# Kernel optimization log

Hardware: AMD Instinct MI355X
Metric: run time of the kernel (lower is better)

## Reference

```python
import jax, jax.numpy as jnp
import numpy as np

B, S, H, NH = 2, 2048, 1024, 16
HD = H // NH


def setup_inputs() -> dict:
    key = jax.random.key(0)
    ks = jax.random.split(key, 12)
    inp = {
        "query": jax.random.normal(ks[0], (B, S, H), dtype=jnp.float32),
        "key": jax.random.normal(ks[1], (B, S, H), dtype=jnp.float32),
        "value": jax.random.normal(ks[2], (B, S, H), dtype=jnp.float32),
        "mask": jnp.ones((B, 1, S, S), dtype=jnp.int32),
        "script_mask": jax.random.uniform(ks[3], (B, S, S), dtype=jnp.float32),
    }
    scale = 1.0 / np.sqrt(H)
    inp["Wq"] = jax.random.normal(ks[4], (H, H), dtype=jnp.float32) * scale
    inp["bq"] = jnp.zeros((H,), dtype=jnp.float32)
    inp["Wk"] = jax.random.normal(ks[5], (H, H), dtype=jnp.float32) * scale
    inp["bk"] = jnp.zeros((H,), dtype=jnp.float32)
    inp["Wv"] = jax.random.normal(ks[6], (H, H), dtype=jnp.float32) * scale
    inp["bv"] = jnp.zeros((H,), dtype=jnp.float32)
    inp["Wo"] = jax.random.normal(ks[7], (H, H), dtype=jnp.float32) * scale
    inp["bo"] = jnp.zeros((H,), dtype=jnp.float32)
    return inp


def reference(query, key, value, mask, script_mask, Wq, bq, Wk, bk, Wv, bv, Wo, bo):
    b, s, h = query.shape
    # projections; torch Linear: x @ W.T + b
    q = (query @ Wq.T + bq).reshape(b, s, NH, HD).transpose(0, 2, 1, 3)  # [b,nh,s,hd]
    k = (key @ Wk.T + bk).reshape(b, s, NH, HD).transpose(0, 2, 1, 3)
    v = (value @ Wv.T + bv).reshape(b, s, NH, HD).transpose(0, 2, 1, 3)
    scores = jnp.einsum("bhqd,bhkd->bhqk", q, k) / jnp.sqrt(jnp.float32(HD))
    # multiplicative script mask, broadcast over heads
    scores = scores * script_mask[:, None, :, :]
    # additive mask: positions where mask == 0 -> -inf
    scores = jnp.where(mask == 0, -jnp.inf, scores)
    attn = jax.nn.softmax(scores, axis=-1)
    out = jnp.einsum("bhqk,bhkd->bhqd", attn, v)  # [b,nh,s,hd]
    out = out.transpose(0, 2, 1, 3).reshape(b, s, h)
    return out @ Wo.T + bo
```

## Files before the change

kernel.cpp:

```cpp
#include <hip/hip_runtime.h>
#include <stdint.h>

#define NH 16
#define SEQ 2048
#define HDIM 1024

typedef short bf16x8 __attribute__((ext_vector_type(8)));
typedef float f32x4 __attribute__((ext_vector_type(4)));

#define NEG_BIG (-1.0e30f)

static __device__ __forceinline__ float bf2f(uint32_t u) {
  union { uint32_t u; float f; } v; v.u = u << 16; return v.f;
}
static __device__ __forceinline__ uint32_t cvtpk_bf16(float lo, float hi) {
  uint32_t r;
  asm("v_cvt_pk_bf16_f32 %0, %1, %2" : "=v"(r) : "v"(lo), "v"(hi));
  return r;
}
static __device__ __forceinline__ uint16_t f2bf(float f) {
  return (uint16_t)cvtpk_bf16(f, f);
}
static __device__ __forceinline__ void gload_lds16(const void* g, void* l) {
  __builtin_amdgcn_global_load_lds(
      (const __attribute__((address_space(1))) void*)g,
      (__attribute__((address_space(3))) void*)l, 16, 0, 0);
}

struct CvtArgs {
  const float* src[7];
  uint16_t* dst[7];
  int nblk[7];
};
__global__ __launch_bounds__(256) void cvt_bf16(CvtArgs a) {
  int ten = blockIdx.y;
  if (blockIdx.x >= a.nblk[ten]) return;
  size_t idx = ((size_t)blockIdx.x * 256 + threadIdx.x) * 8;
  const float* s = a.src[ten] + idx;
  float4 f0 = *(const float4*)(s);
  float4 f1 = *(const float4*)(s + 4);
  uint4 o;
  o.x = cvtpk_bf16(f0.x, f0.y);
  o.y = cvtpk_bf16(f0.z, f0.w);
  o.z = cvtpk_bf16(f1.x, f1.y);
  o.w = cvtpk_bf16(f1.z, f1.w);
  *(uint4*)(a.dst[ten] + idx) = o;
}

__global__ __launch_bounds__(256) void cm_prep(const int4* __restrict__ mask,
                                               const float4* __restrict__ sm,
                                               uint4* __restrict__ cm) {
  int i = blockIdx.x * 256 + threadIdx.x;
  int4 m0 = mask[2 * i];
  int4 m1 = mask[2 * i + 1];
  float4 s0 = sm[2 * i];
  float4 s1 = sm[2 * i + 1];
  const float cst = 0.18033688011112042f;
  auto pk = [&](int mA, int mB, float fa, float fb) -> uint32_t {
    float a = mA ? fa * cst : -1.0f;
    float b = mB ? fb * cst : -1.0f;
    return cvtpk_bf16(a, b);
  };
  uint4 o;
  o.x = pk(m0.x, m0.y, s0.x, s0.y);
  o.y = pk(m0.z, m0.w, s0.z, s0.w);
  o.z = pk(m1.x, m1.y, s1.x, s1.y);
  o.w = pk(m1.z, m1.w, s1.z, s1.w);
  cm[i] = o;
}

struct GemmArgs {
  const uint16_t* A[4];
  const uint16_t* B[4];
  const float* bias[4];
  void* C[4];
};

__global__ __launch_bounds__(256) void gemm_bt(GemmArgs ga, int modeBase) {
  int mode = modeBase + blockIdx.y;
  const uint16_t* __restrict__ A = ga.A[mode];
  const uint16_t* __restrict__ Bm = ga.B[mode];
  const float* __restrict__ bias = ga.bias[mode];

  int bid = blockIdx.x;
  int tm, tn;
  if (mode == 2) { tm = bid & 7; tn = bid >> 3; }
  else           { tm = bid >> 3; tn = bid & 7; }

  __shared__ uint16_t As[3][128 * 32];
  __shared__ uint16_t Bs[3][128 * 32];

  int t = threadIdx.x;
  int lane = t & 63, w = t >> 6;
  int quad = lane >> 4, lm = lane & 15;
  int wm = w >> 1, wn = w & 1;

  const uint16_t* Ab = A + (size_t)tm * 128 * 1024;
  const uint16_t* Bb = Bm + (size_t)tn * 128 * 1024;

  int srow = lane >> 2;
  int scol = (lane & 3) * 8;
  const uint16_t* gA0 = Ab + (size_t)(w * 32 + srow) * 1024 + scol;
  const uint16_t* gA1 = gA0 + 16 * 1024;
  const uint16_t* gB0 = Bb + (size_t)(w * 32 + srow) * 1024 + scol;
  const uint16_t* gB1 = gB0 + 16 * 1024;

  uint16_t* rdA = As[0]; uint16_t* stA = As[1]; uint16_t* nxA = As[2];
  uint16_t* rdB = Bs[0]; uint16_t* stB = Bs[1]; uint16_t* nxB = Bs[2];
  int woff = w * 1024;

  auto STAGE = [&](uint16_t* dA, uint16_t* dB) {
    gload_lds16(gA0, dA + woff);
    gload_lds16(gA1, dA + woff + 512);
    gload_lds16(gB0, dB + woff);
    gload_lds16(gB1, dB + woff + 512);
    gA0 += 32; gA1 += 32; gB0 += 32; gB1 += 32;
  };

  f32x4 acc[4][4] = {};

  STAGE(rdA, rdB);

  for (int kk = 0; kk < 1024; kk += 32) {
    if (kk + 32 < 1024) {
      STAGE(stA, stB);
      asm volatile("s_waitcnt vmcnt(4)" ::: "memory");
    } else {
      asm volatile("s_waitcnt vmcnt(0)" ::: "memory");
    }
    __builtin_amdgcn_s_barrier();
    __builtin_amdgcn_sched_barrier(0);

    bf16x8 af[4], bfr[4];
#pragma unroll
    for (int i = 0; i < 4; i++)
      af[i] = *(const bf16x8*)&rdA[(wm * 64 + i * 16 + lm) * 32 + quad * 8];
#pragma unroll
    for (int j = 0; j < 4; j++)
      bfr[j] = *(const bf16x8*)&rdB[(wn * 64 + j * 16 + lm) * 32 + quad * 8];
#pragma unroll
    for (int i = 0; i < 4; i++)
#pragma unroll
      for (int j = 0; j < 4; j++)
        acc[i][j] = __builtin_amdgcn_mfma_f32_16x16x32_bf16(af[i], bfr[j], acc[i][j], 0, 0, 0);

    uint16_t* tA = rdA; rdA = stA; stA = nxA; nxA = tA;
    uint16_t* tB = rdB; rdB = stB; stB = nxB; nxB = tB;
  }

  int rowb = tm * 128 + wm * 64;
  int colb = tn * 128 + wn * 64;
#pragma unroll
  for (int i = 0; i < 4; i++) {
#pragma unroll
    for (int j = 0; j < 4; j++) {
      int col = colb + j * 16 + lm;
#pragma unroll
      for (int r = 0; r < 4; r++) {
        int row = rowb + i * 16 + quad * 4 + r;
        float v = acc[i][j][r];
        if (mode == 2) {
          v += bias[row];
          int hh = row >> 6, hd = row & 63, b = col >> 11, s2 = col & 2047;
          ((uint16_t*)ga.C[2])[((size_t)((b * NH + hh) * 64 + hd) << 11) + s2] = f2bf(v);
        } else if (mode == 3) {
          v += bias[col];
          ((float*)ga.C[3])[(size_t)row * 1024 + col] = v;
        } else {
          v += bias[col];
          int b = row >> 11, s2 = row & 2047, hh = col >> 6, hd = col & 63;
          ((uint16_t*)ga.C[mode])[(((size_t)(b * NH + hh) * 2048 + s2) << 6) + hd] = f2bf(v);
        }
      }
    }
  }
}

#define LDK 72

__global__ __launch_bounds__(256) void attn(const uint16_t* __restrict__ qp,
                                            const uint16_t* __restrict__ kp,
                                            const uint16_t* __restrict__ vt,
                                            const uint16_t* __restrict__ cm,
                                            uint16_t* __restrict__ ao) {
  int h = blockIdx.x, qt = blockIdx.y, b = blockIdx.z;
  int t = threadIdx.x;
  int lane = t & 63, w = t >> 6;
  int quad = lane >> 4, c = lane & 15;

  __shared__ uint16_t Ks[64 * LDK];
  __shared__ uint16_t VTs[64 * LDK];
  __shared__ uint16_t Ps[64 * LDK];

  size_t bh = (size_t)(b * NH + h);
  const uint16_t* Kb = kp + bh * (SEQ * 64);
  const uint16_t* Vb = vt + bh * (64 * SEQ);
  const uint16_t* CMb = cm + ((size_t)b * SEQ + qt * 64) * SEQ;

  int qrow = qt * 64 + w * 16 + c;
  const uint16_t* Qb = qp + bh * (SEQ * 64) + (size_t)qrow * 64;
  bf16x8 qf0 = *(const bf16x8*)(Qb + quad * 8);
  bf16x8 qf1 = *(const bf16x8*)(Qb + 32 + quad * 8);

  f32x4 Oacc[4] = {};
  float m_run = NEG_BIG;
  float l_run = 0.0f;

  int krow = w * 8 + (lane >> 3);
  int kc = (lane & 7) * 8;

  const uint16_t* pK0 = Kb + (size_t)krow * 64 + kc;
  const uint16_t* pK1 = pK0 + 32 * 64;
  const uint16_t* pV0 = Vb + (size_t)krow * SEQ + kc;
  const uint16_t* pV1 = pV0 + (size_t)32 * SEQ;
  const uint16_t* pCM = CMb + (size_t)(w * 16 + c) * SEQ + quad * 4;

  uint16_t* sK0 = &Ks[krow * LDK + kc];
  uint16_t* sK1 = sK0 + 32 * LDK;
  uint16_t* sV0 = &VTs[krow * LDK + kc];
  uint16_t* sV1 = sV0 + 32 * LDK;

  const uint16_t* rK = &Ks[c * LDK];
  const uint16_t* rV = &VTs[c * LDK];
  uint16_t* sP = &Ps[(w * 16 + c) * LDK];
  int qo = quad * 8;

  for (int kt = 0; kt < SEQ; kt += 64) {
    uint2 cm0 = *(const uint2*)(pCM);
    uint2 cm1 = *(const uint2*)(pCM + 16);
    uint2 cm2 = *(const uint2*)(pCM + 32);
    uint2 cm3 = *(const uint2*)(pCM + 48);
    uint4 k0  = *(const uint4*)(pK0);
    uint4 k1  = *(const uint4*)(pK1);
    uint4 v0g = *(const uint4*)(pV0);
    uint4 v1g = *(const uint4*)(pV1);
    pCM += 64; pK0 += 64 * 64; pK1 += 64 * 64; pV0 += 64; pV1 += 64;
    __syncthreads();
    *(uint4*)sK0 = k0;
    *(uint4*)sK1 = k1;
    *(uint4*)sV0 = v0g;
    *(uint4*)sV1 = v1g;
    __syncthreads();

    f32x4 st[4];
    __builtin_amdgcn_s_setprio(1);
#pragma unroll
    for (int i = 0; i < 4; i++) {
      bf16x8 a0 = *(const bf16x8*)(rK + i * 16 * LDK + qo);
      bf16x8 a1 = *(const bf16x8*)(rK + i * 16 * LDK + 32 + qo);
      f32x4 z = {};
      z = __builtin_amdgcn_mfma_f32_16x16x32_bf16(a0, qf0, z, 0, 0, 0);
      st[i] = __builtin_amdgcn_mfma_f32_16x16x32_bf16(a1, qf1, z, 0, 0, 0);
    }
    __builtin_amdgcn_s_setprio(0);

    float p[16];
    float tmax = NEG_BIG;
    uint2 cmv[4] = {cm0, cm1, cm2, cm3};
#pragma unroll
    for (int i = 0; i < 4; i++) {
      uint32_t w0 = cmv[i].x, w1 = cmv[i].y;
      float cf[4];
      cf[0] = __builtin_bit_cast(float, w0 << 16);
      cf[1] = __builtin_bit_cast(float, w0 & 0xffff0000u);
      cf[2] = __builtin_bit_cast(float, w1 << 16);
      cf[3] = __builtin_bit_cast(float, w1 & 0xffff0000u);
#pragma unroll
      for (int r = 0; r < 4; r++) {
        float sv = st[i][r] * cf[r];
        sv = (cf[r] < 0.0f) ? NEG_BIG : sv;
        p[i * 4 + r] = sv;
      }
      tmax = fmaxf(tmax,
                   fmaxf(fmaxf(p[i * 4 + 0], p[i * 4 + 1]),
                         fmaxf(p[i * 4 + 2], p[i * 4 + 3])));
    }
    tmax = fmaxf(tmax, __shfl_xor(tmax, 16));
    tmax = fmaxf(tmax, __shfl_xor(tmax, 32));
    if (!__all(tmax <= m_run + 8.0f)) {
      float m_new = fmaxf(m_run, tmax);
      float alpha = exp2f(m_run - m_new);
      m_run = m_new;
      l_run *= alpha;
#pragma unroll
      for (int i = 0; i < 4; i++) Oacc[i] *= alpha;
    }
    float ls = 0.0f;
#pragma unroll
    for (int z2 = 0; z2 < 16; z2++) {
      p[z2] = exp2f(p[z2] - m_run);
      ls += p[z2];
    }
    l_run += ls;

#pragma unroll
    for (int i = 0; i < 4; i++) {
      uint2 pkd;
      pkd.x = cvtpk_bf16(p[i * 4 + 0], p[i * 4 + 1]);
      pkd.y = cvtpk_bf16(p[i * 4 + 2], p[i * 4 + 3]);
      *(uint2*)(sP + i * 16 + quad * 4) = pkd;
    }
    asm volatile("s_waitcnt lgkmcnt(0)" ::: "memory");
    __builtin_amdgcn_sched_barrier(0);

    bf16x8 pf0 = *(const bf16x8*)(sP + qo);
    bf16x8 pf1 = *(const bf16x8*)(sP + 32 + qo);
    __builtin_amdgcn_s_setprio(1);
#pragma unroll
    for (int i = 0; i < 4; i++) {
      bf16x8 v0 = *(const bf16x8*)(rV + i * 16 * LDK + qo);
      bf16x8 v1 = *(const bf16x8*)(rV + i * 16 * LDK + 32 + qo);
      Oacc[i] = __builtin_amdgcn_mfma_f32_16x16x32_bf16(v0, pf0, Oacc[i], 0, 0, 0);
      Oacc[i] = __builtin_amdgcn_mfma_f32_16x16x32_bf16(v1, pf1, Oacc[i], 0, 0, 0);
    }
    __builtin_amdgcn_s_setprio(0);
  }

  float lf = l_run + __shfl_xor(l_run, 16);
  lf = lf + __shfl_xor(lf, 32);
  float inv = 1.0f / lf;
  uint16_t* Ob = ao + ((size_t)(b * SEQ) + qt * 64 + w * 16 + c) * HDIM + h * 64;
#pragma unroll
  for (int i = 0; i < 4; i++) {
    uint2 ov;
    ov.x = cvtpk_bf16(Oacc[i][0] * inv, Oacc[i][1] * inv);
    ov.y = cvtpk_bf16(Oacc[i][2] * inv, Oacc[i][3] * inv);
    *(uint2*)(Ob + i * 16 + quad * 4) = ov;
  }
}

extern "C" void kernel_launch(void* const* d_in, const int* in_sizes, int n_in,
                              void* d_out, int out_size, void* d_ws, size_t ws_size,
                              hipStream_t stream) {
  (void)in_sizes; (void)n_in; (void)out_size; (void)ws_size;
  const float* query = (const float*)d_in[0];
  const float* key   = (const float*)d_in[1];
  const float* value = (const float*)d_in[2];
  const int*   mask  = (const int*)d_in[3];
  const float* smask = (const float*)d_in[4];
  const float* Wq = (const float*)d_in[5];
  const float* bq = (const float*)d_in[6];
  const float* Wk = (const float*)d_in[7];
  const float* bk = (const float*)d_in[8];
  const float* Wv = (const float*)d_in[9];
  const float* bv = (const float*)d_in[10];
  const float* Wo = (const float*)d_in[11];
  const float* bo = (const float*)d_in[12];

  char* p = (char*)d_ws;
  uint16_t* xq  = (uint16_t*)p; p += (size_t)2 * SEQ * HDIM * 2;
  uint16_t* xk  = (uint16_t*)p; p += (size_t)2 * SEQ * HDIM * 2;
  uint16_t* xv  = (uint16_t*)p; p += (size_t)2 * SEQ * HDIM * 2;
  uint16_t* wqb = (uint16_t*)p; p += (size_t)HDIM * HDIM * 2;
  uint16_t* wkb = (uint16_t*)p; p += (size_t)HDIM * HDIM * 2;
  uint16_t* wvb = (uint16_t*)p; p += (size_t)HDIM * HDIM * 2;
  uint16_t* wob = (uint16_t*)p; p += (size_t)HDIM * HDIM * 2;
  uint16_t* qp  = (uint16_t*)p; p += (size_t)2 * NH * SEQ * 64 * 2;
  uint16_t* kpp = (uint16_t*)p; p += (size_t)2 * NH * SEQ * 64 * 2;
  uint16_t* vtp = (uint16_t*)p; p += (size_t)2 * NH * SEQ * 64 * 2;
  uint16_t* cmw = (uint16_t*)p; p += (size_t)2 * SEQ * SEQ * 2;
  uint16_t* aob = (uint16_t*)p; p += (size_t)2 * SEQ * HDIM * 2;

  CvtArgs ca;
  ca.src[0] = query; ca.dst[0] = xq;  ca.nblk[0] = 2048;
  ca.src[1] = key;   ca.dst[1] = xk;  ca.nblk[1] = 2048;
  ca.src[2] = value; ca.dst[2] = xv;  ca.nblk[2] = 2048;
  ca.src[3] = Wq;    ca.dst[3] = wqb; ca.nblk[3] = 512;
  ca.src[4] = Wk;    ca.dst[4] = wkb; ca.nblk[4] = 512;
  ca.src[5] = Wv;    ca.dst[5] = wvb; ca.nblk[5] = 512;
  ca.src[6] = Wo;    ca.dst[6] = wob; ca.nblk[6] = 512;
  cvt_bf16<<<dim3(2048, 7), 256, 0, stream>>>(ca);

  cm_prep<<<4096, 256, 0, stream>>>((const int4*)mask, (const float4*)smask, (uint4*)cmw);

  GemmArgs ga;
  ga.A[0] = xq;  ga.B[0] = wqb; ga.bias[0] = bq; ga.C[0] = qp;
  ga.A[1] = xk;  ga.B[1] = wkb; ga.bias[1] = bk; ga.C[1] = kpp;
  ga.A[2] = wvb; ga.B[2] = xv;  ga.bias[2] = bv; ga.C[2] = vtp;
  ga.A[3] = aob; ga.B[3] = wob; ga.bias[3] = bo; ga.C[3] = d_out;

  gemm_bt<<<dim3(256, 3), 256, 0, stream>>>(ga, 0);
  attn<<<dim3(NH, SEQ / 64, 2), 256, 0, stream>>>(qp, kpp, vtp, cmw, aob);
  gemm_bt<<<dim3(256, 1), 256, 0, stream>>>(ga, 3);
}
```

Baseline: 343.2 us.

## Double-buffer K/V tiles in attention and add smaller-tile output GEMM

The attention kernel now double-buffers its K and V shared-memory tiles. The next tile's global loads are issued before the current tile's compute and written to the alternate buffer afterward, which leaves one barrier per iteration instead of two. The output projection moves to a dedicated kernel with 64x128 tiles and 512 blocks, raising occupancy across CUs for the 4096x1024 GEMM. The cost is more LDS per attention block, which may reduce occupancy, and more registers held across the loop.

```diff
diff --git a/kernel.cpp b/kernel.cpp
--- a/kernel.cpp
+++ b/kernel.cpp
@@ -10,9 +10,6 @@
 
 #define NEG_BIG (-1.0e30f)
 
-static __device__ __forceinline__ float bf2f(uint32_t u) {
-  union { uint32_t u; float f; } v; v.u = u << 16; return v.f;
-}
 static __device__ __forceinline__ uint32_t cvtpk_bf16(float lo, float hi) {
   uint32_t r;
   asm("v_cvt_pk_bf16_f32 %0, %1, %2" : "=v"(r) : "v"(lo), "v"(hi));
@@ -163,9 +160,6 @@
           v += bias[row];
           int hh = row >> 6, hd = row & 63, b = col >> 11, s2 = col & 2047;
           ((uint16_t*)ga.C[2])[((size_t)((b * NH + hh) * 64 + hd) << 11) + s2] = f2bf(v);
-        } else if (mode == 3) {
-          v += bias[col];
-          ((float*)ga.C[3])[(size_t)row * 1024 + col] = v;
         } else {
           v += bias[col];
           int b = row >> 11, s2 = row & 2047, hh = col >> 6, hd = col & 63;
@@ -176,7 +170,93 @@
   }
 }
 
+__global__ __launch_bounds__(256) void gemm_out(const uint16_t* __restrict__ A,
+                                                const uint16_t* __restrict__ Bm,
+                                                const float* __restrict__ bias,
+                                                float* __restrict__ C) {
+  int bid = blockIdx.x;
+  int tm = bid >> 3;
+  int tn = bid & 7;
+
+  __shared__ uint16_t As[3][64 * 32];
+  __shared__ uint16_t Bs[3][128 * 32];
+
+  int t = threadIdx.x;
+  int lane = t & 63, w = t >> 6;
+  int quad = lane >> 4, lm = lane & 15;
+  int wm = w >> 1, wn = w & 1;
+
+  const uint16_t* Ab = A + (size_t)tm * 64 * 1024;
+  const uint16_t* Bb = Bm + (size_t)tn * 128 * 1024;
+
+  int srow = lane >> 2;
+  int scol = (lane & 3) * 8;
+  const uint16_t* gA0 = Ab + (size_t)(w * 16 + srow) * 1024 + scol;
+  const uint16_t* gB0 = Bb + (size_t)(w * 32 + srow) * 1024 + scol;
+  const uint16_t* gB1 = gB0 + 16 * 1024;
+
+  uint16_t* rdA = As[0]; uint16_t* stA = As[1]; uint16_t* nxA = As[2];
+  uint16_t* rdB = Bs[0]; uint16_t* stB = Bs[1]; uint16_t* nxB = Bs[2];
+  int woffA = w * 512;
+  int woffB = w * 1024;
+
+  auto STAGE = [&](uint16_t* dA, uint16_t* dB) {
+    gload_lds16(gA0, dA + woffA);
+    gload_lds16(gB0, dB + woffB);
+    gload_lds16(gB1, dB + woffB + 512);
+    gA0 += 32; gB0 += 32; gB1 += 32;
+  };
+
+  f32x4 acc[2][4] = {};
+
+  STAGE(rdA, rdB);
+
+  for (int kk = 0; kk < 1024; kk += 32) {
+    if (kk + 32 < 1024) {
+      STAGE(stA, stB);
+      asm volatile("s_waitcnt vmcnt(3)" ::: "memory");
+    } else {
+      asm volatile("s_waitcnt vmcnt(0)" ::: "memory");
+    }
+    __builtin_amdgcn_s_barrier();
+    __builtin_amdgcn_sched_barrier(0);
+
+    bf16x8 af[2], bfr[4];
+#pragma unroll
+    for (int i = 0; i < 2; i++)
+      af[i] = *(const bf16x8*)&rdA[(wm * 32 + i * 16 + lm) * 32 + quad * 8];
+#pragma unroll
+    for (int j = 0; j < 4; j++)
+      bfr[j] = *(const bf16x8*)&rdB[(wn * 64 + j * 16 + lm) * 32 + quad * 8];
+#pragma unroll
+    for (int i = 0; i < 2; i++)
+#pragma unroll
+      for (int j = 0; j < 4; j++)
+        acc[i][j] = __builtin_amdgcn_mfma_f32_16x16x32_bf16(af[i], bfr[j], acc[i][j], 0, 0, 0);
+
+    uint16_t* tA = rdA; rdA = stA; stA = nxA; nxA = tA;
+    uint16_t* tB = rdB; rdB = stB; stB = nxB; nxB = tB;
+  }
+
+  int rowb = tm * 64 + wm * 32;
+  int colb = tn * 128 + wn * 64;
+#pragma unroll
+  for (int i = 0; i < 2; i++) {
+#pragma unroll
+    for (int j = 0; j < 4; j++) {
+      int col = colb + j * 16 + lm;
+      float bv = bias[col];
+#pragma unroll
+      for (int r = 0; r < 4; r++) {
+        int row = rowb + i * 16 + quad * 4 + r;
+        C[(size_t)row * 1024 + col] = acc[i][j][r] + bv;
+      }
+    }
+  }
+}
+
 #define LDK 72
+#define KVBUF (64 * LDK)
 
 __global__ __launch_bounds__(256) void attn(const uint16_t* __restrict__ qp,
                                             const uint16_t* __restrict__ kp,
@@ -188,9 +268,9 @@
   int lane = t & 63, w = t >> 6;
   int quad = lane >> 4, c = lane & 15;
 
-  __shared__ uint16_t Ks[64 * LDK];
-  __shared__ uint16_t VTs[64 * LDK];
-  __shared__ uint16_t Ps[64 * LDK];
+  __shared__ uint16_t Ks[2 * KVBUF];
+  __shared__ uint16_t VTs[2 * KVBUF];
+  __shared__ uint16_t Ps[KVBUF];
 
   size_t bh = (size_t)(b * NH + h);
   const uint16_t* Kb = kp + bh * (SEQ * 64);
@@ -225,29 +305,46 @@
   uint16_t* sP = &Ps[(w * 16 + c) * LDK];
   int qo = quad * 8;
 
+  {
+    uint4 k0  = *(const uint4*)(pK0);
+    uint4 k1  = *(const uint4*)(pK1);
+    uint4 v0g = *(const uint4*)(pV0);
+    uint4 v1g = *(const uint4*)(pV1);
+    pK0 += 64 * 64; pK1 += 64 * 64; pV0 += 64; pV1 += 64;
+    *(uint4*)sK0 = k0;
+    *(uint4*)sK1 = k1;
+    *(uint4*)sV0 = v0g;
+    *(uint4*)sV1 = v1g;
+    asm volatile("s_waitcnt lgkmcnt(0)" ::: "memory");
+    __builtin_amdgcn_s_barrier();
+  }
+
+  int X = 0;
   for (int kt = 0; kt < SEQ; kt += 64) {
     uint2 cm0 = *(const uint2*)(pCM);
     uint2 cm1 = *(const uint2*)(pCM + 16);
     uint2 cm2 = *(const uint2*)(pCM + 32);
     uint2 cm3 = *(const uint2*)(pCM + 48);
-    uint4 k0  = *(const uint4*)(pK0);
-    uint4 k1  = *(const uint4*)(pK1);
-    uint4 v0g = *(const uint4*)(pV0);
-    uint4 v1g = *(const uint4*)(pV1);
-    pCM += 64; pK0 += 64 * 64; pK1 += 64 * 64; pV0 += 64; pV1 += 64;
-    __syncthreads();
-    *(uint4*)sK0 = k0;
-    *(uint4*)sK1 = k1;
-    *(uint4*)sV0 = v0g;
-    *(uint4*)sV1 = v1g;
-    __syncthreads();
+    pCM += 64;
+    bool more = (kt + 64 < SEQ);
+    uint4 k0, k1, v0g, v1g;
+    if (more) {
+      k0  = *(const uint4*)(pK0);
+      k1  = *(const uint4*)(pK1);
+      v0g = *(const uint4*)(pV0);
+      v1g = *(const uint4*)(pV1);
+      pK0 += 64 * 64; pK1 += 64 * 64; pV0 += 64; pV1 += 64;
+    }
+
+    const uint16_t* rKX = rK + X * KVBUF;
+    const uint16_t* rVX = rV + X * KVBUF;
 
     f32x4 st[4];
     __builtin_amdgcn_s_setprio(1);
 #pragma unroll
     for (int i = 0; i < 4; i++) {
-      bf16x8 a0 = *(const bf16x8*)(rK + i * 16 * LDK + qo);
-      bf16x8 a1 = *(const bf16x8*)(rK + i * 16 * LDK + 32 + qo);
+      bf16x8 a0 = *(const bf16x8*)(rKX + i * 16 * LDK + qo);
+      bf16x8 a1 = *(const bf16x8*)(rKX + i * 16 * LDK + 32 + qo);
       f32x4 z = {};
       z = __builtin_amdgcn_mfma_f32_16x16x32_bf16(a0, qf0, z, 0, 0, 0);
       st[i] = __builtin_amdgcn_mfma_f32_16x16x32_bf16(a1, qf1, z, 0, 0, 0);
@@ -308,12 +405,23 @@
     __builtin_amdgcn_s_setprio(1);
 #pragma unroll
     for (int i = 0; i < 4; i++) {
-      bf16x8 v0 = *(const bf16x8*)(rV + i * 16 * LDK + qo);
-      bf16x8 v1 = *(const bf16x8*)(rV + i * 16 * LDK + 32 + qo);
+      bf16x8 v0 = *(const bf16x8*)(rVX + i * 16 * LDK + qo);
+      bf16x8 v1 = *(const bf16x8*)(rVX + i * 16 * LDK + 32 + qo);
       Oacc[i] = __builtin_amdgcn_mfma_f32_16x16x32_bf16(v0, pf0, Oacc[i], 0, 0, 0);
       Oacc[i] = __builtin_amdgcn_mfma_f32_16x16x32_bf16(v1, pf1, Oacc[i], 0, 0, 0);
     }
     __builtin_amdgcn_s_setprio(0);
+
+    if (more) {
+      int Y = X ^ 1;
+      *(uint4*)(sK0 + Y * KVBUF) = k0;
+      *(uint4*)(sK1 + Y * KVBUF) = k1;
+      *(uint4*)(sV0 + Y * KVBUF) = v0g;
+      *(uint4*)(sV1 + Y * KVBUF) = v1g;
+      asm volatile("s_waitcnt lgkmcnt(0)" ::: "memory");
+      __builtin_amdgcn_s_barrier();
+      X = Y;
+    }
   }
 
   float lf = l_run + __shfl_xor(l_run, 16);
@@ -381,5 +489,5 @@
 
   gemm_bt<<<dim3(256, 3), 256, 0, stream>>>(ga, 0);
   attn<<<dim3(NH, SEQ / 64, 2), 256, 0, stream>>>(qp, kpp, vtp, cmw, aob);
-  gemm_bt<<<dim3(256, 1), 256, 0, stream>>>(ga, 3);
-}
+  gemm_out<<<512, 256, 0, stream>>>(aob, wob, bo, (float*)d_out);
+}
```

Measured after the change: 358.8 us. +4.5%, slower.
